# Optimization experiments

Hardware: AMD Instinct MI355X
Metric: run time of the kernel (lower is better)

The kernel has to match this reference:

```python
import jax, jax.numpy as jnp
import numpy as np

# ----- Cl(3,0,1) projective geometric algebra tables (e0^2=0, e1..e3^2=+1) -----
_BLADES = [(), (0,), (1,), (2,), (3,),
           (0, 1), (0, 2), (0, 3), (1, 2), (1, 3), (2, 3),
           (0, 1, 2), (0, 1, 3), (0, 2, 3), (1, 2, 3),
           (0, 1, 2, 3)]
_IDX = {b: i for i, b in enumerate(_BLADES)}

def _blade_mul(a, b):
    lst = list(a) + list(b); sign = 1; n = len(lst)
    for _ in range(n):
        for j in range(n - 1):
            if lst[j] > lst[j + 1]:
                lst[j], lst[j + 1] = lst[j + 1], lst[j]; sign = -sign
    out, i = [], 0
    while i < len(lst):
        if i + 1 < len(lst) and lst[i] == lst[i + 1]:
            if lst[i] == 0:
                return 0, ()
            i += 2
        else:
            out.append(lst[i]); i += 1
    return sign, tuple(out)

_GPn = np.zeros((16, 16, 16), dtype=np.float32)
for _i, _a in enumerate(_BLADES):
    for _j, _b in enumerate(_BLADES):
        _s, _c = _blade_mul(_a, _b)
        if _s:
            _GPn[_i, _j, _IDX[_c]] = _s
GP = jnp.asarray(_GPn)                       # geometric-product structure constants
_gr = np.array([len(b) for b in _BLADES])
_P = np.stack([np.diag((_gr == g).astype(np.float32)) for g in range(5)])  # grade projections
_L0 = _GPn[1].T                               # left-multiplication by e0
BASIS = jnp.asarray(np.concatenate([_P, np.stack([_L0 @ _P[g] for g in range(4)])], 0))  # (9,16,16) equivariant-linear basis
INNER = jnp.asarray(np.array([0.0 if 0 in b else 1.0 for b in _BLADES], np.float32))    # invariant inner-product mask (8 ones)

N_HEADS = 8
_EPS = 1e-6

def equi_linear(mv, s, wmv, wsm, wms, wss):
    # mv: (..., Cin, 16), s: (..., Sin); scalars couple to the grade-0 component
    y_mv = jnp.einsum('oik,kab,...ib->...oa', wmv, BASIS, mv)
    y_mv = y_mv.at[..., 0].add(jnp.einsum('oi,...i->...o', wsm, s))
    y_s = jnp.einsum('oi,...i->...o', wss, s) + jnp.einsum('oi,...i->...o', wms, mv[..., 0])
    return y_mv, y_s

def equi_ln(mv, s):
    f = jnp.mean(jnp.sum(mv * mv * INNER, -1), -1, keepdims=True)  # mean channel norm
    mv = mv / jnp.sqrt(f + _EPS)[..., None]
    s = s / jnp.sqrt(jnp.mean(s * s, -1, keepdims=True) + _EPS)
    return mv, s

def attention(mv, s, wmv, wsm, wms, wss, womv, wosm, woms, woss):
    B, N, C, _ = mv.shape; S = s.shape[-1]; H = N_HEADS
    qkv_mv, qkv_s = equi_linear(mv, s, wmv, wsm, wms, wss)
    q_mv, k_mv, v_mv = [t.reshape(B, N, H, C // H, 16) for t in jnp.split(qkv_mv, 3, axis=-2)]
    q_s, k_s, v_s = [t.reshape(B, N, H, S // H) for t in jnp.split(qkv_s, 3, axis=-1)]
    scale = 1.0 / np.sqrt(8 * (C // H) + S // H)  # 8 invariant comps per mv channel
    scores = (jnp.einsum('bnhci,bmhci->bhnm', q_mv * INNER, k_mv)
              + jnp.einsum('bnhd,bmhd->bhnm', q_s, k_s)) * scale
    a = jax.nn.softmax(scores, axis=-1)
    o_mv = jnp.einsum('bhnm,bmhci->bnhci', a, v_mv).reshape(B, N, C, 16)
    o_s = jnp.einsum('bhnm,bmhd->bnhd', a, v_s).reshape(B, N, S)
    return equi_linear(o_mv, o_s, womv, wosm, woms, woss)

def geo_mlp(mv, s, w1mv, w1sm, w1ms, w1ss, w2mv, w2sm, w2ms, w2ss):
    C = mv.shape[-2]; S = s.shape[-1]
    h_mv, h_s = equi_linear(mv, s, w1mv, w1sm, w1ms, w1ss)  # (...,2C,16), (...,2S)
    gp = jnp.einsum('ijk,...ci,...cj->...ck', GP, h_mv[..., :C, :], h_mv[..., C:, :])
    gp = gp * jax.nn.gelu(gp[..., :1])                       # scalar-gated nonlinearity
    sh = h_s[..., :S] * jax.nn.gelu(h_s[..., S:])
    return equi_linear(gp, sh, w2mv, w2sm, w2ms, w2ss)

def _forward(inputs, win_mv, win_ms, win_bs,
             a_qkv_wmv, a_qkv_wsm, a_qkv_wms, a_qkv_wss,
             a_out_wmv, a_out_wsm, a_out_wms, a_out_wss,
             m1_wmv, m1_wsm, m1_wms, m1_wss,
             m2_wmv, m2_wsm, m2_wms, m2_wss,
             wout_mv, wout_sm):
    B, N, _ = inputs.shape
    # embed_point: coordinates -> trivector components, homogeneous e123 = 1
    mv0 = jnp.zeros((B, N, 1, 16), inputs.dtype)
    mv0 = mv0.at[..., 14].set(1.0)
    mv0 = mv0.at[..., 13].set(-inputs[..., 0:1])
    mv0 = mv0.at[..., 12].set(inputs[..., 1:2])
    mv0 = mv0.at[..., 11].set(-inputs[..., 2:3])
    mv = jnp.einsum('oik,kab,...ib->...oa', win_mv, BASIS, mv0)  # (B,N,C,16)
    s = jnp.einsum('oi,...i->...o', win_ms, mv0[..., 0]) + win_bs  # (B,N,S)
    L = a_qkv_wmv.shape[0]
    for l in range(L):  # loop over structurally-distinct layers only
        n_mv, n_s = equi_ln(mv, s)
        d_mv, d_s = attention(n_mv, n_s, a_qkv_wmv[l], a_qkv_wsm[l], a_qkv_wms[l], a_qkv_wss[l],
                              a_out_wmv[l], a_out_wsm[l], a_out_wms[l], a_out_wss[l])
        mv, s = mv + d_mv, s + d_s
        n_mv, n_s = equi_ln(mv, s)
        d_mv, d_s = geo_mlp(n_mv, n_s, m1_wmv[l], m1_wsm[l], m1_wms[l], m1_wss[l],
                            m2_wmv[l], m2_wsm[l], m2_wms[l], m2_wss[l])
        mv, s = mv + d_mv, s + d_s
    out_mv = jnp.einsum('oik,kab,...ib->...oa', wout_mv, BASIS, mv)  # (B,N,1,16)
    out_mv = out_mv.at[..., 0].add(jnp.einsum('oi,...i->...o', wout_sm, s))
    nodewise = out_mv[..., 0:1]                 # extract_scalar: (B,N,1,1)
    return jnp.mean(nodewise, axis=(-3, -2))    # mean over (points, channels) -> (B,1)

def setup_inputs() -> dict:
    key = jax.random.key(0)
    B, N, C, S, L = 8, 1024, 16, 32, 8
    ks = iter(jax.random.split(key, 32))
    def p(shape, fan):
        return jax.random.normal(next(ks), shape, jnp.float32) / np.sqrt(fan)
    return {
        'inputs': jax.random.normal(next(ks), (B, N, 3), jnp.float32),
        'win_mv': p((C, 1, 9), 9.0),
        'win_ms': p((S, 1), 1.0),
        'win_bs': p((S,), 1.0),
        'a_qkv_wmv': p((L, 3 * C, C, 9), 9.0 * C),
        'a_qkv_wsm': p((L, 3 * C, S), S),
        'a_qkv_wms': p((L, 3 * S, C), C),
        'a_qkv_wss': p((L, 3 * S, S), S),
        'a_out_wmv': p((L, C, C, 9), 9.0 * C),
        'a_out_wsm': p((L, C, S), S),
        'a_out_wms': p((L, S, C), C),
        'a_out_wss': p((L, S, S), S),
        'm1_wmv': p((L, 2 * C, C, 9), 9.0 * C),
        'm1_wsm': p((L, 2 * C, S), S),
        'm1_wms': p((L, 2 * S, C), C),
        'm1_wss': p((L, 2 * S, S), S),
        'm2_wmv': p((L, C, C, 9), 9.0 * C),
        'm2_wsm': p((L, C, S), S),
        'm2_wms': p((L, S, C), C),
        'm2_wss': p((L, S, S), S),
        'wout_mv': p((1, C, 9), 9.0 * C),
        'wout_sm': p((1, S), S),
    }

def reference(inputs, win_mv, win_ms, win_bs,
              a_qkv_wmv, a_qkv_wsm, a_qkv_wms, a_qkv_wss,
              a_out_wmv, a_out_wsm, a_out_wms, a_out_wss,
              m1_wmv, m1_wsm, m1_wms, m1_wss,
              m2_wmv, m2_wsm, m2_wms, m2_wss,
              wout_mv, wout_sm):
    return _forward(inputs, win_mv, win_ms, win_bs,
                    a_qkv_wmv, a_qkv_wsm, a_qkv_wms, a_qkv_wss,
                    a_out_wmv, a_out_wsm, a_out_wms, a_out_wss,
                    m1_wmv, m1_wsm, m1_wms, m1_wss,
                    m2_wmv, m2_wsm, m2_wms, m2_wss,
                    wout_mv, wout_sm)
```

## Files before the change

kernel.cpp:

```cpp
#include <hip/hip_runtime.h>
#include <math.h>

#define BB 8
#define NN 1024
#define LLAYERS 8

typedef unsigned short ushort_t;
typedef unsigned int uint_t;
using bf16x8 = __attribute__((ext_vector_type(8))) short;
using f32x4  = __attribute__((ext_vector_type(4))) float;

__constant__ int d_GRADE[16] = {0,1,1,1,1,2,2,2,2,2,2,3,3,3,3,4};
__constant__ int d_PAIR[16]  = {-1,0,-1,-1,-1,2,3,4,-1,-1,-1,8,9,10,-1,14};
__constant__ int d_IB[8] = {0,2,3,4,8,9,10,14};
__constant__ int d_I2M[16] = {0,1,2,4,8,3,5,9,6,10,12,7,11,13,14,15};
__constant__ int d_M2I[16] = {0,1,2,5,3,6,8,11,4,7,9,12,10,13,14,15};

#define QSCALE (0.22360679774997896f * 1.4426950408889634f)

__device__ __forceinline__ float gelu_tanh(float x) {
  float y = 0.7978845608028654f * (x + 0.044715f * x * x * x);
  float e2 = __builtin_amdgcn_exp2f(y * -2.8853900817779268f);
  return x * __builtin_amdgcn_rcpf(1.0f + e2);
}

__device__ __forceinline__ ushort_t f2b(float f) {
  union { float f; unsigned int u; } x;
  x.f = f;
  unsigned int r = x.u + 0x7fffu + ((x.u >> 16) & 1u);
  return (ushort_t)(r >> 16);
}

__global__ void __launch_bounds__(256) k_embed(
    const float* __restrict__ inp, const float* __restrict__ win_mv,
    const float* __restrict__ win_ms, const float* __restrict__ win_bs,
    float* __restrict__ mv, float* __restrict__ s)
{
  int tok = blockIdx.x, t = threadIdx.x;
  float x = inp[tok * 3 + 0];
  float y = inp[tok * 3 + 1];
  float z = inp[tok * 3 + 2];
  int o = t >> 4, aa = t & 15;
  float ma = (aa == 14) ? 1.f : (aa == 13) ? -x : (aa == 12) ? y : (aa == 11) ? -z : 0.f;
  int g = d_GRADE[aa];
  float val = win_mv[o * 9 + g] * ma;
  int pr = d_PAIR[aa];
  if (pr >= 0) {
    float mp = (pr == 14) ? 1.f : 0.f;
    val += win_mv[o * 9 + 4 + g] * mp;
  }
  mv[(size_t)tok * 256 + t] = val;
  if (t < 32) s[(size_t)tok * 32 + t] = win_bs[t];
  (void)win_ms;
}

__global__ void __launch_bounds__(256) k_ln_qkv(
    const float* __restrict__ mv, const float* __restrict__ s,
    const float* __restrict__ wmv, const float* __restrict__ wsm,
    const float* __restrict__ wms, const float* __restrict__ wss,
    ushort_t* __restrict__ q_bf, ushort_t* __restrict__ k_bf, ushort_t* __restrict__ vT)
{
  __shared__ float pool[9600];
  float* xmv = pool;
  float* xs  = pool + 2048;
  float* yst = pool + 2304;
  float* sst = pool + 8832;

  int t = threadIdx.x;
  int tok0 = blockIdx.x * 8;
  int b = tok0 >> 10, n0 = tok0 & 1023;
  int a = t & 15, og = t >> 4;
  int g = d_GRADE[a], pr = d_PAIR[a];

  float wgq[16], wpq[16], wgk[16], wpk[16], wgv[16], wpv[16];
  #pragma unroll
  for (int i = 0; i < 16; ++i) {
    wgq[i] = wmv[(og)      * 144 + i * 9 + g];
    wgk[i] = wmv[(16 + og) * 144 + i * 9 + g];
    wgv[i] = wmv[(32 + og) * 144 + i * 9 + g];
    wpq[i] = wmv[(og)      * 144 + i * 9 + 4 + g];
    wpk[i] = wmv[(16 + og) * 144 + i * 9 + 4 + g];
    wpv[i] = wmv[(32 + og) * 144 + i * 9 + 4 + g];
  }

  #pragma unroll
  for (int j = 0; j < 2; ++j)
    *(float4*)&xmv[t * 4 + j * 1024] = *(const float4*)&mv[(size_t)tok0 * 256 + t * 4 + j * 1024];
  if (t < 64)
    *(float4*)&xs[t * 4] = *(const float4*)&s[(size_t)tok0 * 32 + t * 4];
  __syncthreads();

  if (t < 128) {
    int tk = t >> 4, ch = t & 15;
    float* xp = &xmv[tk * 256 + ch * 16];
    float4 v0 = *(float4*)&xp[0], v1 = *(float4*)&xp[4];
    float4 v2 = *(float4*)&xp[8], v3 = *(float4*)&xp[12];
    float ss = v0.x*v0.x + v0.z*v0.z + v0.w*v0.w + v1.x*v1.x
             + v2.x*v2.x + v2.y*v2.y + v2.z*v2.z + v3.z*v3.z;
    ss += __shfl_xor(ss, 1); ss += __shfl_xor(ss, 2);
    ss += __shfl_xor(ss, 4); ss += __shfl_xor(ss, 8);
    float inv = rsqrtf(ss / 16.f + 1e-6f);
    v0.x*=inv; v0.y*=inv; v0.z*=inv; v0.w*=inv;
    v1.x*=inv; v1.y*=inv; v1.z*=inv; v1.w*=inv;
    v2.x*=inv; v2.y*=inv; v2.z*=inv; v2.w*=inv;
    v3.x*=inv; v3.y*=inv; v3.z*=inv; v3.w*=inv;
    *(float4*)&xp[0] = v0; *(float4*)&xp[4] = v1;
    *(float4*)&xp[8] = v2; *(float4*)&xp[12] = v3;
    float s0 = xs[tk * 32 + ch * 2], s1 = xs[tk * 32 + ch * 2 + 1];
    float s2 = s0 * s0 + s1 * s1;
    s2 += __shfl_xor(s2, 1); s2 += __shfl_xor(s2, 2);
    s2 += __shfl_xor(s2, 4); s2 += __shfl_xor(s2, 8);
    float sinv = rsqrtf(s2 / 32.f + 1e-6f);
    xs[tk * 32 + ch * 2] = s0 * sinv;
    xs[tk * 32 + ch * 2 + 1] = s1 * sinv;
  }
  __syncthreads();

  for (int tk = 0; tk < 8; ++tk) {
    float y0 = 0.f, y1 = 0.f, y2 = 0.f;
    const float* xb = &xmv[tk * 256];
    #pragma unroll
    for (int i = 0; i < 16; ++i) {
      float xa_ = xb[i * 16 + a];
      y0 += wgq[i] * xa_; y1 += wgk[i] * xa_; y2 += wgv[i] * xa_;
    }
    if (pr >= 0) {
      #pragma unroll
      for (int i = 0; i < 16; ++i) {
        float xp_ = xb[i * 16 + pr];
        y0 += wpq[i] * xp_; y1 += wpk[i] * xp_; y2 += wpv[i] * xp_;
      }
    }
    yst[(tk * 48 + og) * 17 + a] = y0;
    yst[(tk * 48 + 16 + og) * 17 + a] = y1;
    yst[(tk * 48 + 32 + og) * 17 + a] = y2;
  }
  __syncthreads();

  for (int u = t; u < 384; u += 256) {
    int tk = u / 48, o = u % 48;
    float add = 0.f;
    #pragma unroll
    for (int j = 0; j < 32; ++j) add += wsm[o * 32 + j] * xs[tk * 32 + j];
    yst[(tk * 48 + o) * 17 + 0] += add;
  }
  for (int u = t; u < 768; u += 256) {
    int tk = u / 96, o96 = u % 96;
    float yy = 0.f;
    #pragma unroll
    for (int j = 0; j < 32; ++j) yy += wss[o96 * 32 + j] * xs[tk * 32 + j];
    #pragma unroll
    for (int i = 0; i < 16; ++i) yy += wms[o96 * 16 + i] * xmv[tk * 256 + i * 16];
    sst[tk * 96 + o96] = yy;
  }
  __syncthreads();

  if (t < 128) {
    int isK = t >> 6;
    int r = t & 63;
    int tk = r >> 3, h = r & 7;
    float scale = isK ? 1.f : QSCALE;
    const float* base = &yst[(tk * 48 + isK * 16) * 17];
    ushort_t tmp[32];
    #pragma unroll
    for (int j = 0; j < 8; ++j) {
      int blade = d_IB[j];
      tmp[j]     = f2b(base[(2 * h)     * 17 + blade] * scale);
      tmp[8 + j] = f2b(base[(2 * h + 1) * 17 + blade] * scale);
    }
    #pragma unroll
    for (int d = 0; d < 4; ++d)
      tmp[16 + d] = f2b(sst[tk * 96 + isK * 32 + h * 4 + d] * scale);
    #pragma unroll
    for (int j2 = 20; j2 < 32; ++j2) tmp[j2] = 0;
    uint_t out[16];
    #pragma unroll
    for (int j3 = 0; j3 < 16; ++j3)
      out[j3] = (uint_t)tmp[2 * j3] | ((uint_t)tmp[2 * j3 + 1] << 16);
    ushort_t* dst = (isK ? k_bf : q_bf) + ((size_t)(b * 8 + h) * 1024 + n0 + tk) * 32;
    *(uint4*)(dst +  0) = make_uint4(out[0],  out[1],  out[2],  out[3]);
    *(uint4*)(dst +  8) = make_uint4(out[4],  out[5],  out[6],  out[7]);
    *(uint4*)(dst + 16) = make_uint4(out[8],  out[9],  out[10], out[11]);
    *(uint4*)(dst + 24) = make_uint4(out[12], out[13], out[14], out[15]);
  }
  {
    int h = t >> 5, dim = t & 31;
    int ch = 2 * h + (dim >> 4), blade = dim & 15;
    uint_t ov[4];
    #pragma unroll
    for (int tk = 0; tk < 8; ++tk) {
      ushort_t bv = f2b(yst[(tk * 48 + 32 + ch) * 17 + blade]);
      if (tk & 1) ov[tk >> 1] |= ((uint_t)bv) << 16; else ov[tk >> 1] = bv;
    }
    ushort_t* dst = vT + ((size_t)(b * 8 + h) * 48 + dim) * 1024 + n0;
    *(uint4*)dst = make_uint4(ov[0], ov[1], ov[2], ov[3]);
  }
  if (t < 32) {
    int h = t >> 2, d = t & 3;
    uint_t ov[4];
    #pragma unroll
    for (int tk = 0; tk < 8; ++tk) {
      ushort_t bv = f2b(sst[tk * 96 + 64 + h * 4 + d]);
      if (tk & 1) ov[tk >> 1] |= ((uint_t)bv) << 16; else ov[tk >> 1] = bv;
    }
    ushort_t* dst = vT + ((size_t)(b * 8 + h) * 48 + 32 + d) * 1024 + n0;
    *(uint4*)dst = make_uint4(ov[0], ov[1], ov[2], ov[3]);
  }
  if (t < 8) {
    ushort_t* dst = vT + ((size_t)(b * 8 + t) * 48 + 36) * 1024 + n0;
    *(uint4*)dst = make_uint4(0x3F803F80u, 0x3F803F80u, 0x3F803F80u, 0x3F803F80u);
  }
}

#define OPART_STRIDE 2359296
#define LPART_STRIDE 65536
__global__ void __launch_bounds__(256) k_attn(
    const ushort_t* __restrict__ q_bf, const ushort_t* __restrict__ k_bf,
    const ushort_t* __restrict__ vT, float* __restrict__ o_mvA, float* __restrict__ lA)
{
  __shared__ __align__(16) ushort_t kst[64 * 40];
  __shared__ __align__(16) ushort_t vst[48 * 72];
  __shared__ __align__(16) ushort_t plds[4][1280];
  int bx = blockIdx.x;
  int bh = bx & 63, qg = bx >> 6;
  int qb = qg & 15, kg = qg >> 4;
  int b = bh >> 3, h = bh & 7;
  int t = threadIdx.x;
  int w = t >> 6, lane = t & 63;
  int quad = lane >> 4, col = lane & 15;
  int q16 = qb * 64 + w * 16;
  size_t hb = (size_t)bh * 1024;
  ushort_t* myp = &plds[w][0];

  float* o_mvp = o_mvA + (size_t)kg * OPART_STRIDE;
  float* o_sp  = o_mvp + 2097152;
  float* l_p   = lA + (size_t)kg * LPART_STRIDE;

  bf16x8 qfrag = *(const bf16x8*)(q_bf + (hb + q16 + col) * 32 + quad * 8);

  f32x4 ot0 = {0.f,0.f,0.f,0.f}, ot1 = {0.f,0.f,0.f,0.f}, ot2 = {0.f,0.f,0.f,0.f};

  const ushort_t* kbase = k_bf + hb * 32;
  const ushort_t* vbase = vT + (size_t)bh * 48 * 1024;
  int k0 = kg * 512;

  int skey = t >> 2, sc4 = t & 3;
  for (int kt = 0; kt < 8; ++kt) {
    int kb = k0 + kt * 64;
    __syncthreads();
    *(uint4*)&kst[skey * 40 + sc4 * 8] =
        *(const uint4*)(kbase + (size_t)(kb + skey) * 32 + sc4 * 8);
    for (int u = t; u < 296; u += 256) {
      int row = u >> 3, c8 = u & 7;
      *(uint4*)&vst[row * 72 + c8 * 8] =
          *(const uint4*)(vbase + (size_t)row * 1024 + kb + c8 * 8);
    }
    __syncthreads();

    bf16x8 sk0 = *(const bf16x8*)&kst[(     col) * 40 + quad * 8];
    bf16x8 sk1 = *(const bf16x8*)&kst[(16 + col) * 40 + quad * 8];
    bf16x8 sk2 = *(const bf16x8*)&kst[(32 + col) * 40 + quad * 8];
    bf16x8 sk3 = *(const bf16x8*)&kst[(48 + col) * 40 + quad * 8];
    bf16x8 va0 = *(const bf16x8*)&vst[(     col) * 72 + quad * 8];
    bf16x8 va1 = *(const bf16x8*)&vst[(16 + col) * 72 + quad * 8];
    bf16x8 va2 = *(const bf16x8*)&vst[(32 + col) * 72 + quad * 8];
    bf16x8 vb0 = *(const bf16x8*)&vst[(     col) * 72 + 32 + quad * 8];
    bf16x8 vb1 = *(const bf16x8*)&vst[(16 + col) * 72 + 32 + quad * 8];
    bf16x8 vb2 = *(const bf16x8*)&vst[(32 + col) * 72 + 32 + quad * 8];
    f32x4 zero = {0.f,0.f,0.f,0.f};
    f32x4 sa0 = __builtin_amdgcn_mfma_f32_16x16x32_bf16(sk0, qfrag, zero, 0, 0, 0);
    f32x4 sa1 = __builtin_amdgcn_mfma_f32_16x16x32_bf16(sk1, qfrag, zero, 0, 0, 0);
    f32x4 sb0 = __builtin_amdgcn_mfma_f32_16x16x32_bf16(sk2, qfrag, zero, 0, 0, 0);
    f32x4 sb1 = __builtin_amdgcn_mfma_f32_16x16x32_bf16(sk3, qfrag, zero, 0, 0, 0);

    union { float f; uint_t u; } e0, e1, e2, e3;
    e0.f = __builtin_amdgcn_exp2f(sa0[0]); e1.f = __builtin_amdgcn_exp2f(sa0[1]);
    e2.f = __builtin_amdgcn_exp2f(sa0[2]); e3.f = __builtin_amdgcn_exp2f(sa0[3]);
    uint_t a0 = __builtin_amdgcn_perm(e1.u, e0.u, 0x07060302u);
    uint_t a1 = __builtin_amdgcn_perm(e3.u, e2.u, 0x07060302u);
    e0.f = __builtin_amdgcn_exp2f(sa1[0]); e1.f = __builtin_amdgcn_exp2f(sa1[1]);
    e2.f = __builtin_amdgcn_exp2f(sa1[2]); e3.f = __builtin_amdgcn_exp2f(sa1[3]);
    uint_t a2 = __builtin_amdgcn_perm(e1.u, e0.u, 0x07060302u);
    uint_t a3 = __builtin_amdgcn_perm(e3.u, e2.u, 0x07060302u);
    e0.f = __builtin_amdgcn_exp2f(sb0[0]); e1.f = __builtin_amdgcn_exp2f(sb0[1]);
    e2.f = __builtin_amdgcn_exp2f(sb0[2]); e3.f = __builtin_amdgcn_exp2f(sb0[3]);
    uint_t b0 = __builtin_amdgcn_perm(e1.u, e0.u, 0x07060302u);
    uint_t b1 = __builtin_amdgcn_perm(e3.u, e2.u, 0x07060302u);
    e0.f = __builtin_amdgcn_exp2f(sb1[0]); e1.f = __builtin_amdgcn_exp2f(sb1[1]);
    e2.f = __builtin_amdgcn_exp2f(sb1[2]); e3.f = __builtin_amdgcn_exp2f(sb1[3]);
    uint_t b2 = __builtin_amdgcn_perm(e1.u, e0.u, 0x07060302u);
    uint_t b3 = __builtin_amdgcn_perm(e3.u, e2.u, 0x07060302u);

    *(uint2*)(myp + col * 40 + quad * 4)            = make_uint2(a0, a1);
    *(uint2*)(myp + col * 40 + 16 + quad * 4)       = make_uint2(a2, a3);
    *(uint2*)(myp + 640 + col * 40 + quad * 4)      = make_uint2(b0, b1);
    *(uint2*)(myp + 640 + col * 40 + 16 + quad * 4) = make_uint2(b2, b3);
    __builtin_amdgcn_wave_barrier();
    bf16x8 pfa = *(const bf16x8*)(myp + col * 40 + quad * 8);
    bf16x8 pfb = *(const bf16x8*)(myp + 640 + col * 40 + quad * 8);
    __builtin_amdgcn_wave_barrier();
    ot0 = __builtin_amdgcn_mfma_f32_16x16x32_bf16(va0, pfa, ot0, 0, 0, 0);
    ot1 = __builtin_amdgcn_mfma_f32_16x16x32_bf16(va1, pfa, ot1, 0, 0, 0);
    ot2 = __builtin_amdgcn_mfma_f32_16x16x32_bf16(va2, pfa, ot2, 0, 0, 0);
    ot0 = __builtin_amdgcn_mfma_f32_16x16x32_bf16(vb0, pfb, ot0, 0, 0, 0);
    ot1 = __builtin_amdgcn_mfma_f32_16x16x32_bf16(vb1, pfb, ot1, 0, 0, 0);
    ot2 = __builtin_amdgcn_mfma_f32_16x16x32_bf16(vb2, pfb, ot2, 0, 0, 0);
  }

  int tok = b * NN + q16 + col;
  float* op0 = o_mvp + (size_t)tok * 256 + (2 * h) * 16 + quad * 4;
  op0[0] = ot0[0]; op0[1] = ot0[1]; op0[2] = ot0[2]; op0[3] = ot0[3];
  float* op1 = o_mvp + (size_t)tok * 256 + (2 * h + 1) * 16 + quad * 4;
  op1[0] = ot1[0]; op1[1] = ot1[1]; op1[2] = ot1[2]; op1[3] = ot1[3];
  if (quad == 0) {
    float* osp = o_sp + (size_t)tok * 32 + h * 4;
    osp[0] = ot2[0]; osp[1] = ot2[1]; osp[2] = ot2[2]; osp[3] = ot2[3];
  }
  if (quad == 1) l_p[hb + q16 + col] = ot2[0];
}

__global__ void __launch_bounds__(256) k_out_res(
    const float* __restrict__ o_mvA, const float* __restrict__ lA,
    const float* __restrict__ wmv, const float* __restrict__ wsm,
    const float* __restrict__ wms, const float* __restrict__ wss,
    float* __restrict__ mv, float* __restrict__ s)
{
  __shared__ float pool[4544];
  float* xo    = pool;
  float* xso   = pool + 2048;
  float* yst   = pool + 2304;
  float* invls = pool + 4480;

  const float* o_sA  = o_mvA + 2097152;
  const float* o_mvB = o_mvA + OPART_STRIDE;
  const float* o_sB  = o_mvB + 2097152;
  const float* lB    = lA + LPART_STRIDE;

  int t = threadIdx.x;
  int tok0 = blockIdx.x * 8;
  int b8 = (tok0 >> 10) * 8, n0 = tok0 & 1023;
  int a = t & 15, og = t >> 4;
  int g = d_GRADE[a], pr = d_PAIR[a];

  float wg[16], wp[16];
  #pragma unroll
  for (int i = 0; i < 16; ++i) {
    wg[i] = wmv[og * 144 + i * 9 + g];
    wp[i] = wmv[og * 144 + i * 9 + 4 + g];
  }

  float4 ra[2], rc[2];
  #pragma unroll
  for (int j = 0; j < 2; ++j) {
    ra[j] = *(const float4*)&o_mvA[(size_t)tok0 * 256 + t * 4 + j * 1024];
    rc[j] = *(const float4*)&o_mvB[(size_t)tok0 * 256 + t * 4 + j * 1024];
  }
  float4 sa4 = {0,0,0,0}, sc4 = {0,0,0,0};
  if (t < 64) {
    int tk = t >> 3, h = t & 7;
    sa4 = *(const float4*)&o_sA[(size_t)(tok0 + tk) * 32 + h * 4];
    sc4 = *(const float4*)&o_sB[(size_t)(tok0 + tk) * 32 + h * 4];
    float la = lA[(size_t)(b8 + h) * 1024 + n0 + tk];
    float lb = lB[(size_t)(b8 + h) * 1024 + n0 + tk];
    invls[t] = 1.f / (la + lb);
  }
  __syncthreads();

  #pragma unroll
  for (int j = 0; j < 2; ++j) {
    int idx = t * 4 + j * 1024;
    int tk = idx >> 8, o = (idx >> 4) & 15;
    float il = invls[tk * 8 + (o >> 1)];
    xo[idx + 0] = (ra[j].x + rc[j].x) * il;
    xo[idx + 1] = (ra[j].y + rc[j].y) * il;
    xo[idx + 2] = (ra[j].z + rc[j].z) * il;
    xo[idx + 3] = (ra[j].w + rc[j].w) * il;
  }
  if (t < 64) {
    int tk = t >> 3, h = t & 7;
    float il = invls[t];
    xso[tk * 32 + h * 4 + 0] = (sa4.x + sc4.x) * il;
    xso[tk * 32 + h * 4 + 1] = (sa4.y + sc4.y) * il;
    xso[tk * 32 + h * 4 + 2] = (sa4.z + sc4.z) * il;
    xso[tk * 32 + h * 4 + 3] = (sa4.w + sc4.w) * il;
  }
  __syncthreads();

  for (int tk = 0; tk < 8; ++tk) {
    float y = 0.f;
    const float* xb = &xo[tk * 256];
    #pragma unroll
    for (int i = 0; i < 16; ++i) y += wg[i] * xb[i * 16 + a];
    if (pr >= 0) {
      #pragma unroll
      for (int i = 0; i < 16; ++i) y += wp[i] * xb[i * 16 + pr];
    }
    yst[(tk * 16 + og) * 17 + a] = y;
  }
  __syncthreads();

  if (t < 128) {
    int tk = t >> 4, o = t & 15;
    float add = 0.f;
    #pragma unroll
    for (int j = 0; j < 32; ++j) add += wsm[o * 32 + j] * xso[tk * 32 + j];
    yst[(tk * 16 + o) * 17 + 0] += add;
  }
  {
    int o32 = t & 31, tk = t >> 5;
    float ys = 0.f;
    #pragma unroll
    for (int j = 0; j < 32; ++j) ys += wss[o32 * 32 + j] * xso[tk * 32 + j];
    #pragma unroll
    for (int i = 0; i < 16; ++i) ys += wms[o32 * 16 + i] * xo[tk * 256 + i * 16];
    s[(size_t)(tok0 + tk) * 32 + o32] += ys;
  }
  __syncthreads();

  #pragma unroll
  for (int p = 0; p < 8; ++p) {
    int flat = p * 256 + t;
    int tk = flat >> 8, rem = flat & 255, o = rem >> 4, a2 = rem & 15;
    mv[(size_t)tok0 * 256 + flat] += yst[(tk * 16 + o) * 17 + a2];
  }
}

__global__ void __launch_bounds__(256) k_mlp_res(
    float* __restrict__ mv, float* __restrict__ s,
    const float* __restrict__ w1mv, const float* __restrict__ w1sm,
    const float* __restrict__ w1ms, const float* __restrict__ w1ss,
    const float* __restrict__ w2mv, const float* __restrict__ w2sm,
    const float* __restrict__ w2ms, const float* __restrict__ w2ss)
{
  __shared__ float pool[9600];
  float* xmv  = pool;
  float* xs   = pool + 2048;
  float* hst  = pool + 2304;
  float* y2st = pool + 2304;
  float* hsst = pool + 6656;
  float* gst  = pool + 7168;
  float* shst = pool + 9344;

  int t = threadIdx.x;
  int tok0 = blockIdx.x * 8;
  int a = t & 15, og = t >> 4;
  int g = d_GRADE[a], pr = d_PAIR[a];

  unsigned long long jpack = 0; unsigned int spack = 0, skipm = 0;
  {
    int mk = d_I2M[a];
    for (int i = 0; i < 16; ++i) {
      int mi = d_I2M[i];
      int mj = mi ^ mk;
      if (mi & mj & 1) { skipm |= 1u << i; continue; }
      int j = d_M2I[mj];
      int sw = 0;
      for (int bb2 = 0; bb2 < 4; ++bb2)
        if (mj & (1 << bb2)) sw += __popc(((unsigned)mi) >> (bb2 + 1));
      jpack |= (unsigned long long)j << (4 * i);
      spack |= (unsigned)(sw & 1) << i;
    }
  }

  float wg1a[16], wp1a[16], wg1b[16], wp1b[16];
  #pragma unroll
  for (int i = 0; i < 16; ++i) {
    wg1a[i] = w1mv[(og)      * 144 + i * 9 + g];
    wg1b[i] = w1mv[(16 + og) * 144 + i * 9 + g];
    wp1a[i] = w1mv[(og)      * 144 + i * 9 + 4 + g];
    wp1b[i] = w1mv[(16 + og) * 144 + i * 9 + 4 + g];
  }

  #pragma unroll
  for (int j = 0; j < 2; ++j)
    *(float4*)&xmv[t * 4 + j * 1024] = *(const float4*)&mv[(size_t)tok0 * 256 + t * 4 + j * 1024];
  if (t < 64)
    *(float4*)&xs[t * 4] = *(const float4*)&s[(size_t)tok0 * 32 + t * 4];
  __syncthreads();

  if (t < 128) {
    int tk = t >> 4, ch = t & 15;
    float* xp = &xmv[tk * 256 + ch * 16];
    float4 v0 = *(float4*)&xp[0], v1 = *(float4*)&xp[4];
    float4 v2 = *(float4*)&xp[8], v3 = *(float4*)&xp[12];
    float ss = v0.x*v0.x + v0.z*v0.z + v0.w*v0.w + v1.x*v1.x
             + v2.x*v2.x + v2.y*v2.y + v2.z*v2.z + v3.z*v3.z;
    ss += __shfl_xor(ss, 1); ss += __shfl_xor(ss, 2);
    ss += __shfl_xor(ss, 4); ss += __shfl_xor(ss, 8);
    float inv = rsqrtf(ss / 16.f + 1e-6f);
    v0.x*=inv; v0.y*=inv; v0.z*=inv; v0.w*=inv;
    v1.x*=inv; v1.y*=inv; v1.z*=inv; v1.w*=inv;
    v2.x*=inv; v2.y*=inv; v2.z*=inv; v2.w*=inv;
    v3.x*=inv; v3.y*=inv; v3.z*=inv; v3.w*=inv;
    *(float4*)&xp[0] = v0; *(float4*)&xp[4] = v1;
    *(float4*)&xp[8] = v2; *(float4*)&xp[12] = v3;
    float s0 = xs[tk * 32 + ch * 2], s1 = xs[tk * 32 + ch * 2 + 1];
    float s2 = s0 * s0 + s1 * s1;
    s2 += __shfl_xor(s2, 1); s2 += __shfl_xor(s2, 2);
    s2 += __shfl_xor(s2, 4); s2 += __shfl_xor(s2, 8);
    float sinv = rsqrtf(s2 / 32.f + 1e-6f);
    xs[tk * 32 + ch * 2] = s0 * sinv;
    xs[tk * 32 + ch * 2 + 1] = s1 * sinv;
  }
  __syncthreads();

  for (int tk = 0; tk < 8; ++tk) {
    float y0 = 0.f, y1 = 0.f;
    const float* xb = &xmv[tk * 256];
    #pragma unroll
    for (int i = 0; i < 16; ++i) {
      float xa_ = xb[i * 16 + a];
      y0 += wg1a[i] * xa_; y1 += wg1b[i] * xa_;
    }
    if (pr >= 0) {
      #pragma unroll
      for (int i = 0; i < 16; ++i) {
        float xp_ = xb[i * 16 + pr];
        y0 += wp1a[i] * xp_; y1 += wp1b[i] * xp_;
      }
    }
    hst[(tk * 32 + og) * 17 + a] = y0;
    hst[(tk * 32 + 16 + og) * 17 + a] = y1;
  }
  for (int u = t; u < 512; u += 256) {
    int tk = u >> 6, o64 = u & 63;
    float yy = 0.f;
    #pragma unroll
    for (int j = 0; j < 32; ++j) yy += w1ss[o64 * 32 + j] * xs[tk * 32 + j];
    #pragma unroll
    for (int i = 0; i < 16; ++i) yy += w1ms[o64 * 16 + i] * xmv[tk * 256 + i * 16];
    hsst[tk * 64 + o64] = yy;
  }
  __syncthreads();

  {
    int tk = t >> 5, o = t & 31;
    float add = 0.f;
    #pragma unroll
    for (int j = 0; j < 32; ++j) add += w1sm[o * 32 + j] * xs[tk * 32 + j];
    hst[(tk * 32 + o) * 17 + 0] += add;
  }
  __syncthreads();

  for (int tk = 0; tk < 8; ++tk) {
    const float* h1b = &hst[(tk * 32 + og) * 17];
    const float* h2b = &hst[(tk * 32 + 16 + og) * 17];
    float gacc = 0.f;
    #pragma unroll
    for (int i = 0; i < 16; ++i) {
      int j = (int)((jpack >> (4 * i)) & 15ull);
      float val = h1b[i] * h2b[j];
      float sv = ((spack >> i) & 1) ? -val : val;
      gacc += ((skipm >> i) & 1) ? 0.f : sv;
    }
    float gp0 = __shfl(gacc, (int)(t & 48), 64);
    gst[(tk * 16 + og) * 17 + a] = gacc * gelu_tanh(gp0);
  }
  {
    int tk = t >> 5, o32 = t & 31;
    shst[tk * 32 + o32] = hsst[tk * 64 + o32] * gelu_tanh(hsst[tk * 64 + 32 + o32]);
  }
  __syncthreads();

  {
    float wg2[16], wp2[16];
    #pragma unroll
    for (int i = 0; i < 16; ++i) {
      wg2[i] = w2mv[og * 144 + i * 9 + g];
      wp2[i] = w2mv[og * 144 + i * 9 + 4 + g];
    }
    for (int tk = 0; tk < 8; ++tk) {
      float y = 0.f;
      #pragma unroll
      for (int i = 0; i < 16; ++i) y += wg2[i] * gst[(tk * 16 + i) * 17 + a];
      if (pr >= 0) {
        #pragma unroll
        for (int i = 0; i < 16; ++i) y += wp2[i] * gst[(tk * 16 + i) * 17 + pr];
      }
      y2st[(tk * 16 + og) * 17 + a] = y;
    }
  }
  __syncthreads();

  if (t < 128) {
    int tk = t >> 4, o = t & 15;
    float add = 0.f;
    #pragma unroll
    for (int j = 0; j < 32; ++j) add += w2sm[o * 32 + j] * shst[tk * 32 + j];
    y2st[(tk * 16 + o) * 17 + 0] += add;
  }
  {
    int tk = t >> 5, o32 = t & 31;
    float ys = 0.f;
    #pragma unroll
    for (int j = 0; j < 32; ++j) ys += w2ss[o32 * 32 + j] * shst[tk * 32 + j];
    #pragma unroll
    for (int i = 0; i < 16; ++i) ys += w2ms[o32 * 16 + i] * gst[(tk * 16 + i) * 17 + 0];
    s[(size_t)(tok0 + tk) * 32 + o32] += ys;
  }
  __syncthreads();

  #pragma unroll
  for (int p = 0; p < 8; ++p) {
    int flat = p * 256 + t;
    int tk = flat >> 8, rem = flat & 255, o = rem >> 4, a2 = rem & 15;
    mv[(size_t)tok0 * 256 + flat] += y2st[(tk * 16 + o) * 17 + a2];
  }
}

__global__ void __launch_bounds__(256) k_final(
    const float* __restrict__ mv, const float* __restrict__ s,
    const float* __restrict__ wout_mv, const float* __restrict__ wout_sm,
    float* __restrict__ out)
{
  __shared__ float red[256];
  int b = blockIdx.x, t = threadIdx.x;
  float part = 0.f;
  for (int n = t; n < NN; n += 256) {
    const float* mvp = mv + ((size_t)(b * NN + n) * 16) * 16;
    const float* sp = s + (size_t)(b * NN + n) * 32;
    float acc = 0.f;
    #pragma unroll
    for (int i = 0; i < 16; ++i) acc += wout_mv[i * 9] * mvp[i * 16];
    #pragma unroll
    for (int j = 0; j < 32; ++j) acc += wout_sm[j] * sp[j];
    part += acc;
  }
  red[t] = part;
  __syncthreads();
  for (int w = 128; w > 0; w >>= 1) { if (t < w) red[t] += red[t + w]; __syncthreads(); }
  if (t == 0) out[b] = red[0] / (float)NN;
}

extern "C" void kernel_launch(void* const* d_in, const int* in_sizes, int n_in,
                              void* d_out, int out_size, void* d_ws, size_t ws_size,
                              hipStream_t stream) {
  const float* inputs    = (const float*)d_in[0];
  const float* win_mv    = (const float*)d_in[1];
  const float* win_ms    = (const float*)d_in[2];
  const float* win_bs    = (const float*)d_in[3];
  const float* a_qkv_wmv = (const float*)d_in[4];
  const float* a_qkv_wsm = (const float*)d_in[5];
  const float* a_qkv_wms = (const float*)d_in[6];
  const float* a_qkv_wss = (const float*)d_in[7];
  const float* a_out_wmv = (const float*)d_in[8];
  const float* a_out_wsm = (const float*)d_in[9];
  const float* a_out_wms = (const float*)d_in[10];
  const float* a_out_wss = (const float*)d_in[11];
  const float* m1_wmv    = (const float*)d_in[12];
  const float* m1_wsm    = (const float*)d_in[13];
  const float* m1_wms    = (const float*)d_in[14];
  const float* m1_wss    = (const float*)d_in[15];
  const float* m2_wmv    = (const float*)d_in[16];
  const float* m2_wsm    = (const float*)d_in[17];
  const float* m2_wms    = (const float*)d_in[18];
  const float* m2_wss    = (const float*)d_in[19];
  const float* wout_mv   = (const float*)d_in[20];
  const float* wout_sm   = (const float*)d_in[21];
  float* out = (float*)d_out;

  float* ws = (float*)d_ws;
  float* mv    = ws;
  float* s     = mv + 2097152;
  float* o_mvA = s + 262144;
  float* lA    = o_mvA + 2 * 2359296;
  ushort_t* q_bf = (ushort_t*)(lA + 2 * 65536);
  ushort_t* k_bf = q_bf + 2097152;
  ushort_t* vT   = k_bf + 2097152;

  int ntok = BB * NN;
  int ntile = ntok / 8;
  k_embed<<<ntok, 256, 0, stream>>>(inputs, win_mv, win_ms, win_bs, mv, s);

  for (int l = 0; l < LLAYERS; ++l) {
    k_ln_qkv<<<ntile, 256, 0, stream>>>(mv, s,
        a_qkv_wmv + (size_t)l * 48 * 16 * 9, a_qkv_wsm + (size_t)l * 48 * 32,
        a_qkv_wms + (size_t)l * 96 * 16,     a_qkv_wss + (size_t)l * 96 * 32,
        q_bf, k_bf, vT);
    k_attn<<<2048, 256, 0, stream>>>(q_bf, k_bf, vT, o_mvA, lA);
    k_out_res<<<ntile, 256, 0, stream>>>(o_mvA, lA,
        a_out_wmv + (size_t)l * 16 * 16 * 9, a_out_wsm + (size_t)l * 16 * 32,
        a_out_wms + (size_t)l * 32 * 16,     a_out_wss + (size_t)l * 32 * 32,
        mv, s);
    k_mlp_res<<<ntile, 256, 0, stream>>>(mv, s,
        m1_wmv + (size_t)l * 32 * 16 * 9, m1_wsm + (size_t)l * 32 * 32,
        m1_wms + (size_t)l * 64 * 16,     m1_wss + (size_t)l * 64 * 32,
        m2_wmv + (size_t)l * 16 * 16 * 9, m2_wsm + (size_t)l * 16 * 32,
        m2_wms + (size_t)l * 32 * 16,     m2_wss + (size_t)l * 32 * 32);
  }

  k_final<<<BB, 256, 0, stream>>>(mv, s, wout_mv, wout_sm, out);

  (void)in_sizes; (void)n_in; (void)out_size; (void)ws_size;
}
```

Measured before the change: 1.021 ms.

## Fuse attention output projection and MLP block into one per-tile kernel

Merges the attention out-projection/residual kernel and the LayerNorm+MLP/residual kernel into a single kernel, so the residual stream stays in registers instead of being written to and re-read from global memory. Shared-memory tiles are transposed to a channel-contiguous, padded layout so each dot product reads four float4 vectors rather than strided scalars. LayerNorm now uses a cross-wave shuffle and shared-memory reduction. The cost is more shared memory per block (about 47KB) and more registers, which may reduce occupancy.

```diff
diff --git a/kernel.cpp b/kernel.cpp
--- a/kernel.cpp
+++ b/kernel.cpp
@@ -29,6 +29,19 @@
   x.f = f;
   unsigned int r = x.u + 0x7fffu + ((x.u >> 16) & 1u);
   return (ushort_t)(r >> 16);
+}
+
+__device__ __forceinline__ float dot16_row(const float* __restrict__ row,
+                                           const float* __restrict__ w) {
+  float4 r0 = *(const float4*)(row + 0);
+  float4 r1 = *(const float4*)(row + 4);
+  float4 r2 = *(const float4*)(row + 8);
+  float4 r3 = *(const float4*)(row + 12);
+  float y = r0.x * w[0] + r0.y * w[1] + r0.z * w[2] + r0.w * w[3];
+  y += r1.x * w[4] + r1.y * w[5] + r1.z * w[6] + r1.w * w[7];
+  y += r2.x * w[8] + r2.y * w[9] + r2.z * w[10] + r2.w * w[11];
+  y += r3.x * w[12] + r3.y * w[13] + r3.z * w[14] + r3.w * w[15];
+  return y;
 }
 
 __global__ void __launch_bounds__(256) k_embed(
@@ -319,17 +332,30 @@
   if (quad == 1) l_p[hb + q16 + col] = ot2[0];
 }
 
-__global__ void __launch_bounds__(256) k_out_res(
+__global__ void __launch_bounds__(256) k_post(
     const float* __restrict__ o_mvA, const float* __restrict__ lA,
-    const float* __restrict__ wmv, const float* __restrict__ wsm,
-    const float* __restrict__ wms, const float* __restrict__ wss,
+    const float* __restrict__ womv, const float* __restrict__ wosm,
+    const float* __restrict__ woms, const float* __restrict__ woss,
+    const float* __restrict__ w1mv, const float* __restrict__ w1sm,
+    const float* __restrict__ w1ms, const float* __restrict__ w1ss,
+    const float* __restrict__ w2mv, const float* __restrict__ w2sm,
+    const float* __restrict__ w2ms, const float* __restrict__ w2ss,
     float* __restrict__ mv, float* __restrict__ s)
 {
-  __shared__ float pool[4544];
-  float* xo    = pool;
-  float* xso   = pool + 2048;
-  float* yst   = pool + 2304;
-  float* invls = pool + 4480;
+  __shared__ __align__(16) float pool[11744];
+  float* xoT   = pool;
+  float* gstT  = pool;
+  float* xso   = pool + 2560;
+  float* shst  = pool + 2560;
+  float* invls = pool + 2816;
+  float* w2smT = pool + 2816;
+  float* wsmT  = pool + 2880;
+  float* redp  = pool + 3008;
+  float* xT    = pool + 3040;
+  float* xs    = pool + 5600;
+  float* w1smT = pool + 5856;
+  float* hst   = pool + 6112;
+  float* hsst  = pool + 11232;
 
   const float* o_sA  = o_mvA + 2097152;
   const float* o_mvB = o_mvA + OPART_STRIDE;
@@ -341,110 +367,8 @@
   int b8 = (tok0 >> 10) * 8, n0 = tok0 & 1023;
   int a = t & 15, og = t >> 4;
   int g = d_GRADE[a], pr = d_PAIR[a];
-
-  float wg[16], wp[16];
-  #pragma unroll
-  for (int i = 0; i < 16; ++i) {
-    wg[i] = wmv[og * 144 + i * 9 + g];
-    wp[i] = wmv[og * 144 + i * 9 + 4 + g];
-  }
-
-  float4 ra[2], rc[2];
-  #pragma unroll
-  for (int j = 0; j < 2; ++j) {
-    ra[j] = *(const float4*)&o_mvA[(size_t)tok0 * 256 + t * 4 + j * 1024];
-    rc[j] = *(const float4*)&o_mvB[(size_t)tok0 * 256 + t * 4 + j * 1024];
-  }
-  float4 sa4 = {0,0,0,0}, sc4 = {0,0,0,0};
-  if (t < 64) {
-    int tk = t >> 3, h = t & 7;
-    sa4 = *(const float4*)&o_sA[(size_t)(tok0 + tk) * 32 + h * 4];
-    sc4 = *(const float4*)&o_sB[(size_t)(tok0 + tk) * 32 + h * 4];
-    float la = lA[(size_t)(b8 + h) * 1024 + n0 + tk];
-    float lb = lB[(size_t)(b8 + h) * 1024 + n0 + tk];
-    invls[t] = 1.f / (la + lb);
-  }
-  __syncthreads();
-
-  #pragma unroll
-  for (int j = 0; j < 2; ++j) {
-    int idx = t * 4 + j * 1024;
-    int tk = idx >> 8, o = (idx >> 4) & 15;
-    float il = invls[tk * 8 + (o >> 1)];
-    xo[idx + 0] = (ra[j].x + rc[j].x) * il;
-    xo[idx + 1] = (ra[j].y + rc[j].y) * il;
-    xo[idx + 2] = (ra[j].z + rc[j].z) * il;
-    xo[idx + 3] = (ra[j].w + rc[j].w) * il;
-  }
-  if (t < 64) {
-    int tk = t >> 3, h = t & 7;
-    float il = invls[t];
-    xso[tk * 32 + h * 4 + 0] = (sa4.x + sc4.x) * il;
-    xso[tk * 32 + h * 4 + 1] = (sa4.y + sc4.y) * il;
-    xso[tk * 32 + h * 4 + 2] = (sa4.z + sc4.z) * il;
-    xso[tk * 32 + h * 4 + 3] = (sa4.w + sc4.w) * il;
-  }
-  __syncthreads();
-
-  for (int tk = 0; tk < 8; ++tk) {
-    float y = 0.f;
-    const float* xb = &xo[tk * 256];
-    #pragma unroll
-    for (int i = 0; i < 16; ++i) y += wg[i] * xb[i * 16 + a];
-    if (pr >= 0) {
-      #pragma unroll
-      for (int i = 0; i < 16; ++i) y += wp[i] * xb[i * 16 + pr];
-    }
-    yst[(tk * 16 + og) * 17 + a] = y;
-  }
-  __syncthreads();
-
-  if (t < 128) {
-    int tk = t >> 4, o = t & 15;
-    float add = 0.f;
-    #pragma unroll
-    for (int j = 0; j < 32; ++j) add += wsm[o * 32 + j] * xso[tk * 32 + j];
-    yst[(tk * 16 + o) * 17 + 0] += add;
-  }
-  {
-    int o32 = t & 31, tk = t >> 5;
-    float ys = 0.f;
-    #pragma unroll
-    for (int j = 0; j < 32; ++j) ys += wss[o32 * 32 + j] * xso[tk * 32 + j];
-    #pragma unroll
-    for (int i = 0; i < 16; ++i) ys += wms[o32 * 16 + i] * xo[tk * 256 + i * 16];
-    s[(size_t)(tok0 + tk) * 32 + o32] += ys;
-  }
-  __syncthreads();
-
-  #pragma unroll
-  for (int p = 0; p < 8; ++p) {
-    int flat = p * 256 + t;
-    int tk = flat >> 8, rem = flat & 255, o = rem >> 4, a2 = rem & 15;
-    mv[(size_t)tok0 * 256 + flat] += yst[(tk * 16 + o) * 17 + a2];
-  }
-}
-
-__global__ void __launch_bounds__(256) k_mlp_res(
-    float* __restrict__ mv, float* __restrict__ s,
-    const float* __restrict__ w1mv, const float* __restrict__ w1sm,
-    const float* __restrict__ w1ms, const float* __restrict__ w1ss,
-    const float* __restrict__ w2mv, const float* __restrict__ w2sm,
-    const float* __restrict__ w2ms, const float* __restrict__ w2ss)
-{
-  __shared__ float pool[9600];
-  float* xmv  = pool;
-  float* xs   = pool + 2048;
-  float* hst  = pool + 2304;
-  float* y2st = pool + 2304;
-  float* hsst = pool + 6656;
-  float* gst  = pool + 7168;
-  float* shst = pool + 9344;
-
-  int t = threadIdx.x;
-  int tok0 = blockIdx.x * 8;
-  int a = t & 15, og = t >> 4;
-  int g = d_GRADE[a], pr = d_PAIR[a];
+  int inner_a = ((d_I2M[a] & 1) == 0) ? 1 : 0;
+  int tks = t >> 5, o32 = t & 31;
 
   unsigned long long jpack = 0; unsigned int spack = 0, skipm = 0;
   {
@@ -462,103 +386,191 @@
     }
   }
 
-  float wg1a[16], wp1a[16], wg1b[16], wp1b[16];
-  #pragma unroll
-  for (int i = 0; i < 16; ++i) {
-    wg1a[i] = w1mv[(og)      * 144 + i * 9 + g];
-    wg1b[i] = w1mv[(16 + og) * 144 + i * 9 + g];
-    wp1a[i] = w1mv[(og)      * 144 + i * 9 + 4 + g];
-    wp1b[i] = w1mv[(16 + og) * 144 + i * 9 + 4 + g];
-  }
-
-  #pragma unroll
-  for (int j = 0; j < 2; ++j)
-    *(float4*)&xmv[t * 4 + j * 1024] = *(const float4*)&mv[(size_t)tok0 * 256 + t * 4 + j * 1024];
-  if (t < 64)
-    *(float4*)&xs[t * 4] = *(const float4*)&s[(size_t)tok0 * 32 + t * 4];
+  float4 ra[2], rc[2];
+  #pragma unroll
+  for (int j = 0; j < 2; ++j) {
+    ra[j] = *(const float4*)&o_mvA[(size_t)tok0 * 256 + t * 4 + j * 1024];
+    rc[j] = *(const float4*)&o_mvB[(size_t)tok0 * 256 + t * 4 + j * 1024];
+  }
+  float mvold[8];
+  #pragma unroll
+  for (int tk = 0; tk < 8; ++tk)
+    mvold[tk] = mv[(size_t)(tok0 + tk) * 256 + t];
+  float sold = s[(size_t)(tok0 + tks) * 32 + o32];
+  float4 sa4 = {0,0,0,0}, sc4 = {0,0,0,0};
+  if (t < 64) {
+    int tk = t >> 3, h = t & 7;
+    sa4 = *(const float4*)&o_sA[(size_t)(tok0 + tk) * 32 + h * 4];
+    sc4 = *(const float4*)&o_sB[(size_t)(tok0 + tk) * 32 + h * 4];
+    float la = lA[(size_t)(b8 + h) * 1024 + n0 + tk];
+    float lb = lB[(size_t)(b8 + h) * 1024 + n0 + tk];
+    invls[t] = 1.f / (la + lb);
+  }
+  __syncthreads();
+
+  #pragma unroll
+  for (int j = 0; j < 2; ++j) {
+    int e = t * 4 + j * 1024;
+    int tk = e >> 8, ch = (e >> 4) & 15, bs = e & 15;
+    float il = invls[tk * 8 + (ch >> 1)];
+    xoT[tk * 320 + (bs + 0) * 20 + ch] = (ra[j].x + rc[j].x) * il;
+    xoT[tk * 320 + (bs + 1) * 20 + ch] = (ra[j].y + rc[j].y) * il;
+    xoT[tk * 320 + (bs + 2) * 20 + ch] = (ra[j].z + rc[j].z) * il;
+    xoT[tk * 320 + (bs + 3) * 20 + ch] = (ra[j].w + rc[j].w) * il;
+  }
+  if (t < 64) {
+    int tk = t >> 3, h = t & 7;
+    float il = invls[t];
+    xso[tk * 32 + h * 4 + 0] = (sa4.x + sc4.x) * il;
+    xso[tk * 32 + h * 4 + 1] = (sa4.y + sc4.y) * il;
+    xso[tk * 32 + h * 4 + 2] = (sa4.z + sc4.z) * il;
+    xso[tk * 32 + h * 4 + 3] = (sa4.w + sc4.w) * il;
+  }
   __syncthreads();
 
   if (t < 128) {
-    int tk = t >> 4, ch = t & 15;
-    float* xp = &xmv[tk * 256 + ch * 16];
-    float4 v0 = *(float4*)&xp[0], v1 = *(float4*)&xp[4];
-    float4 v2 = *(float4*)&xp[8], v3 = *(float4*)&xp[12];
-    float ss = v0.x*v0.x + v0.z*v0.z + v0.w*v0.w + v1.x*v1.x
-             + v2.x*v2.x + v2.y*v2.y + v2.z*v2.z + v3.z*v3.z;
-    ss += __shfl_xor(ss, 1); ss += __shfl_xor(ss, 2);
-    ss += __shfl_xor(ss, 4); ss += __shfl_xor(ss, 8);
-    float inv = rsqrtf(ss / 16.f + 1e-6f);
-    v0.x*=inv; v0.y*=inv; v0.z*=inv; v0.w*=inv;
-    v1.x*=inv; v1.y*=inv; v1.z*=inv; v1.w*=inv;
-    v2.x*=inv; v2.y*=inv; v2.z*=inv; v2.w*=inv;
-    v3.x*=inv; v3.y*=inv; v3.z*=inv; v3.w*=inv;
-    *(float4*)&xp[0] = v0; *(float4*)&xp[4] = v1;
-    *(float4*)&xp[8] = v2; *(float4*)&xp[12] = v3;
-    float s0 = xs[tk * 32 + ch * 2], s1 = xs[tk * 32 + ch * 2 + 1];
-    float s2 = s0 * s0 + s1 * s1;
+    int tk = t >> 4, o = t & 15;
+    float add = 0.f;
+    #pragma unroll
+    for (int j = 0; j < 32; ++j) add += wosm[o * 32 + j] * xso[tk * 32 + j];
+    wsmT[tk * 16 + o] = add;
+  }
+  __syncthreads();
+
+  float mvnew[8], sq[8];
+  {
+    float wg[16], wp[16];
+    #pragma unroll
+    for (int i = 0; i < 16; ++i) {
+      wg[i] = womv[og * 144 + i * 9 + g];
+      wp[i] = womv[og * 144 + i * 9 + 4 + g];
+    }
+    #pragma unroll
+    for (int tk = 0; tk < 8; ++tk) {
+      float y = dot16_row(&xoT[tk * 320 + a * 20], wg);
+      if (pr >= 0) y += dot16_row(&xoT[tk * 320 + pr * 20], wp);
+      if (a == 0) y += wsmT[tk * 16 + og];
+      mvnew[tk] = mvold[tk] + y;
+      sq[tk] = inner_a ? mvnew[tk] * mvnew[tk] : 0.f;
+    }
+  }
+  float snew;
+  {
+    float sdel = 0.f;
+    #pragma unroll
+    for (int j = 0; j < 32; ++j) sdel += woss[o32 * 32 + j] * xso[tks * 32 + j];
+    float wm[16];
+    #pragma unroll
+    for (int i = 0; i < 16; ++i) wm[i] = woms[o32 * 16 + i];
+    sdel += dot16_row(&xoT[tks * 320 + 0], wm);
+    snew = sold + sdel;
+  }
+
+  #pragma unroll
+  for (int off = 1; off < 64; off <<= 1) {
+    #pragma unroll
+    for (int tk = 0; tk < 8; ++tk) sq[tk] += __shfl_xor(sq[tk], off);
+  }
+  if ((t & 63) == 0) {
+    #pragma unroll
+    for (int tk = 0; tk < 8; ++tk) redp[(t >> 6) * 8 + tk] = sq[tk];
+  }
+  __syncthreads();
+  #pragma unroll
+  for (int tk = 0; tk < 8; ++tk) {
+    float f = redp[tk] + redp[8 + tk] + redp[16 + tk] + redp[24 + tk];
+    float inv = rsqrtf(f / 16.f + 1e-6f);
+    xT[tk * 320 + a * 20 + og] = mvnew[tk] * inv;
+  }
+  {
+    float s2 = snew * snew;
     s2 += __shfl_xor(s2, 1); s2 += __shfl_xor(s2, 2);
-    s2 += __shfl_xor(s2, 4); s2 += __shfl_xor(s2, 8);
+    s2 += __shfl_xor(s2, 4); s2 += __shfl_xor(s2, 8); s2 += __shfl_xor(s2, 16);
     float sinv = rsqrtf(s2 / 32.f + 1e-6f);
-    xs[tk * 32 + ch * 2] = s0 * sinv;
-    xs[tk * 32 + ch * 2 + 1] = s1 * sinv;
-  }
-  __syncthreads();
-
-  for (int tk = 0; tk < 8; ++tk) {
-    float y0 = 0.f, y1 = 0.f;
-    const float* xb = &xmv[tk * 256];
+    xs[tks * 32 + o32] = snew * sinv;
+  }
+  __syncthreads();
+
+  {
+    float add = 0.f;
+    #pragma unroll
+    for (int j = 0; j < 32; ++j) add += w1sm[o32 * 32 + j] * xs[tks * 32 + j];
+    w1smT[tks * 32 + o32] = add;
+  }
+  __syncthreads();
+
+  {
+    float wg1a[16], wp1a[16], wg1b[16], wp1b[16];
     #pragma unroll
     for (int i = 0; i < 16; ++i) {
-      float xa_ = xb[i * 16 + a];
-      y0 += wg1a[i] * xa_; y1 += wg1b[i] * xa_;
-    }
-    if (pr >= 0) {
-      #pragma unroll
-      for (int i = 0; i < 16; ++i) {
-        float xp_ = xb[i * 16 + pr];
-        y0 += wp1a[i] * xp_; y1 += wp1b[i] * xp_;
+      wg1a[i] = w1mv[(og)      * 144 + i * 9 + g];
+      wg1b[i] = w1mv[(16 + og) * 144 + i * 9 + g];
+      wp1a[i] = w1mv[(og)      * 144 + i * 9 + 4 + g];
+      wp1b[i] = w1mv[(16 + og) * 144 + i * 9 + 4 + g];
+    }
+    #pragma unroll
+    for (int tk = 0; tk < 8; ++tk) {
+      const float* rowa = &xT[tk * 320 + a * 20];
+      float y0 = dot16_row(rowa, wg1a);
+      float y1 = dot16_row(rowa, wg1b);
+      if (pr >= 0) {
+        const float* rowp = &xT[tk * 320 + pr * 20];
+        y0 += dot16_row(rowp, wp1a);
+        y1 += dot16_row(rowp, wp1b);
       }
-    }
-    hst[(tk * 32 + og) * 17 + a] = y0;
-    hst[(tk * 32 + 16 + og) * 17 + a] = y1;
-  }
-  for (int u = t; u < 512; u += 256) {
+      if (a == 0) {
+        y0 += w1smT[tk * 32 + og];
+        y1 += w1smT[tk * 32 + 16 + og];
+      }
+      hst[tk * 640 + og * 20 + a] = y0;
+      hst[tk * 640 + (16 + og) * 20 + a] = y1;
+    }
+  }
+  #pragma unroll
+  for (int p = 0; p < 2; ++p) {
+    int u = p * 256 + t;
     int tk = u >> 6, o64 = u & 63;
     float yy = 0.f;
     #pragma unroll
     for (int j = 0; j < 32; ++j) yy += w1ss[o64 * 32 + j] * xs[tk * 32 + j];
-    #pragma unroll
-    for (int i = 0; i < 16; ++i) yy += w1ms[o64 * 16 + i] * xmv[tk * 256 + i * 16];
+    float wm[16];
+    #pragma unroll
+    for (int i = 0; i < 16; ++i) wm[i] = w1ms[o64 * 16 + i];
+    yy += dot16_row(&xT[tk * 320 + 0], wm);
     hsst[tk * 64 + o64] = yy;
   }
   __syncthreads();
 
-  {
-    int tk = t >> 5, o = t & 31;
-    float add = 0.f;
-    #pragma unroll
-    for (int j = 0; j < 32; ++j) add += w1sm[o * 32 + j] * xs[tk * 32 + j];
-    hst[(tk * 32 + o) * 17 + 0] += add;
-  }
-  __syncthreads();
-
+  #pragma unroll
   for (int tk = 0; tk < 8; ++tk) {
-    const float* h1b = &hst[(tk * 32 + og) * 17];
-    const float* h2b = &hst[(tk * 32 + 16 + og) * 17];
+    const float* row1 = &hst[tk * 640 + og * 20];
+    float4 q0 = *(const float4*)(row1 + 0);
+    float4 q1 = *(const float4*)(row1 + 4);
+    float4 q2 = *(const float4*)(row1 + 8);
+    float4 q3 = *(const float4*)(row1 + 12);
+    float r1[16] = {q0.x,q0.y,q0.z,q0.w, q1.x,q1.y,q1.z,q1.w,
+                    q2.x,q2.y,q2.z,q2.w, q3.x,q3.y,q3.z,q3.w};
+    const float* h2b = &hst[tk * 640 + (16 + og) * 20];
     float gacc = 0.f;
     #pragma unroll
     for (int i = 0; i < 16; ++i) {
       int j = (int)((jpack >> (4 * i)) & 15ull);
-      float val = h1b[i] * h2b[j];
+      float val = r1[i] * h2b[j];
       float sv = ((spack >> i) & 1) ? -val : val;
       gacc += ((skipm >> i) & 1) ? 0.f : sv;
     }
     float gp0 = __shfl(gacc, (int)(t & 48), 64);
-    gst[(tk * 16 + og) * 17 + a] = gacc * gelu_tanh(gp0);
-  }
-  {
-    int tk = t >> 5, o32 = t & 31;
-    shst[tk * 32 + o32] = hsst[tk * 64 + o32] * gelu_tanh(hsst[tk * 64 + 32 + o32]);
+    gstT[tk * 320 + a * 20 + og] = gacc * gelu_tanh(gp0);
+  }
+  shst[tks * 32 + o32] = hsst[tks * 64 + o32] * gelu_tanh(hsst[tks * 64 + 32 + o32]);
+  __syncthreads();
+
+  if (t < 128) {
+    int tk = t >> 4, o = t & 15;
+    float add = 0.f;
+    #pragma unroll
+    for (int j = 0; j < 32; ++j) add += w2sm[o * 32 + j] * shst[tk * 32 + j];
+    w2smT[tk * 16 + o] = add;
   }
   __syncthreads();
 
@@ -569,42 +581,23 @@
       wg2[i] = w2mv[og * 144 + i * 9 + g];
       wp2[i] = w2mv[og * 144 + i * 9 + 4 + g];
     }
+    #pragma unroll
     for (int tk = 0; tk < 8; ++tk) {
-      float y = 0.f;
-      #pragma unroll
-      for (int i = 0; i < 16; ++i) y += wg2[i] * gst[(tk * 16 + i) * 17 + a];
-      if (pr >= 0) {
-        #pragma unroll
-        for (int i = 0; i < 16; ++i) y += wp2[i] * gst[(tk * 16 + i) * 17 + pr];
-      }
-      y2st[(tk * 16 + og) * 17 + a] = y;
-    }
-  }
-  __syncthreads();
-
-  if (t < 128) {
-    int tk = t >> 4, o = t & 15;
-    float add = 0.f;
-    #pragma unroll
-    for (int j = 0; j < 32; ++j) add += w2sm[o * 32 + j] * shst[tk * 32 + j];
-    y2st[(tk * 16 + o) * 17 + 0] += add;
-  }
-  {
-    int tk = t >> 5, o32 = t & 31;
+      float y = dot16_row(&gstT[tk * 320 + a * 20], wg2);
+      if (pr >= 0) y += dot16_row(&gstT[tk * 320 + pr * 20], wp2);
+      if (a == 0) y += w2smT[tk * 16 + og];
+      mv[(size_t)(tok0 + tk) * 256 + t] = mvnew[tk] + y;
+    }
+  }
+  {
     float ys = 0.f;
     #pragma unroll
-    for (int j = 0; j < 32; ++j) ys += w2ss[o32 * 32 + j] * shst[tk * 32 + j];
-    #pragma unroll
-    for (int i = 0; i < 16; ++i) ys += w2ms[o32 * 16 + i] * gst[(tk * 16 + i) * 17 + 0];
-    s[(size_t)(tok0 + tk) * 32 + o32] += ys;
-  }
-  __syncthreads();
-
-  #pragma unroll
-  for (int p = 0; p < 8; ++p) {
-    int flat = p * 256 + t;
-    int tk = flat >> 8, rem = flat & 255, o = rem >> 4, a2 = rem & 15;
-    mv[(size_t)tok0 * 256 + flat] += y2st[(tk * 16 + o) * 17 + a2];
+    for (int j = 0; j < 32; ++j) ys += w2ss[o32 * 32 + j] * shst[tks * 32 + j];
+    float wm[16];
+    #pragma unroll
+    for (int i = 0; i < 16; ++i) wm[i] = w2ms[o32 * 16 + i];
+    ys += dot16_row(&gstT[tks * 320 + 0], wm);
+    s[(size_t)(tok0 + tks) * 32 + o32] = snew + ys;
   }
 }
 
@@ -678,15 +671,14 @@
         a_qkv_wms + (size_t)l * 96 * 16,     a_qkv_wss + (size_t)l * 96 * 32,
         q_bf, k_bf, vT);
     k_attn<<<2048, 256, 0, stream>>>(q_bf, k_bf, vT, o_mvA, lA);
-    k_out_res<<<ntile, 256, 0, stream>>>(o_mvA, lA,
+    k_post<<<ntile, 256, 0, stream>>>(o_mvA, lA,
         a_out_wmv + (size_t)l * 16 * 16 * 9, a_out_wsm + (size_t)l * 16 * 32,
         a_out_wms + (size_t)l * 32 * 16,     a_out_wss + (size_t)l * 32 * 32,
-        mv, s);
-    k_mlp_res<<<ntile, 256, 0, stream>>>(mv, s,
         m1_wmv + (size_t)l * 32 * 16 * 9, m1_wsm + (size_t)l * 32 * 32,
         m1_wms + (size_t)l * 64 * 16,     m1_wss + (size_t)l * 64 * 32,
         m2_wmv + (size_t)l * 16 * 16 * 9, m2_wsm + (size_t)l * 16 * 32,
-        m2_wms + (size_t)l * 32 * 16,     m2_wss + (size_t)l * 32 * 32);
+        m2_wms + (size_t)l * 32 * 16,     m2_wss + (size_t)l * 32 * 32,
+        mv, s);
   }
 
   k_final<<<BB, 256, 0, stream>>>(mv, s, wout_mv, wout_sm, out);
```

Result: slower. 1.102 ms (+7.9%).
